# Performance work log

Measured on AMD Instinct MI355X. Metric: run time of the kernel, lower is better.

The kernel has to match this reference:

```python
import jax, jax.numpy as jnp
import numpy as np

N = 500_000      # total points
B = 64           # graphs in batch
D_IN = 64        # input feature dim (conv.in_tensor_reps.dim)
D_HID = 128      # EdgeConv MLP hidden
D_OUT = 128      # EdgeConv MLP out


def setup_inputs() -> dict:
    key = jax.random.key(0)
    k = jax.random.split(key, 8)
    x = jax.random.normal(k[0], (N, D_IN), jnp.float32)
    pos = jax.random.normal(k[1], (N, 3), jnp.float32)
    batch = jnp.sort(jax.random.randint(k[2], (N,), 0, B, dtype=jnp.int32))
    lframes = jax.random.normal(k[3], (N, 3, 3), jnp.float32)
    fan1 = 2 * D_IN + 3
    W1 = jax.random.normal(k[4], (fan1, D_HID), jnp.float32) / np.sqrt(fan1)
    b1 = jnp.zeros((D_HID,), jnp.float32)
    W2 = jax.random.normal(k[5], (D_HID, D_OUT), jnp.float32) / np.sqrt(D_HID)
    b2 = jnp.zeros((D_OUT,), jnp.float32)
    return {"x": x, "pos": pos, "batch": batch, "lframes": lframes,
            "W1": W1, "b1": b1, "W2": W2, "b2": b2}


def reference(x, pos, batch, lframes, W1, b1, W2, b2):
    n = pos.shape[0]
    # scatter-mean: center of mass per graph
    counts = jax.ops.segment_sum(jnp.ones((n,), pos.dtype), batch, num_segments=B)
    coms = jax.ops.segment_sum(pos, batch, num_segments=B) / jnp.maximum(counts, 1.0)[:, None]
    # distance of each point to its graph's COM
    dist = jnp.linalg.norm(pos - coms[batch], axis=-1)
    # scatter-min argmin per graph (first occurrence, like torch_scatter.scatter_min)
    min_d = jax.ops.segment_min(dist, batch, num_segments=B)
    node_ids = jnp.arange(n, dtype=jnp.int32)
    cand = jnp.where(dist <= min_d[batch], node_ids, n)
    idx = jnp.minimum(jax.ops.segment_min(cand, batch, num_segments=B), n - 1)  # [B]
    # gathers for the destination (center) nodes
    x_dst = x[idx]          # [B, D_IN]
    pos_dst = pos[idx]      # [B, 3]
    lframes_dst = lframes[idx]  # [B, 3, 3]
    # EdgeConv over edge_index = [arange(N) -> batch]:
    # message_e = MLP([x_dst_i, x_src_j - x_dst_i, pos_j - pos_i]), max-aggregated per graph
    xd = x_dst[batch]                      # [N, D_IN]
    feat = jnp.concatenate([xd, x - xd, pos - pos_dst[batch]], axis=-1)  # [N, 2*D_IN+3]
    h = jax.nn.relu(feat @ W1 + b1)        # [N, D_HID]
    msg = h @ W2 + b2                      # [N, D_OUT]
    out = jax.ops.segment_max(msg, batch, num_segments=B)  # [B, D_OUT]
    return out, pos_dst, batch[idx], lframes_dst
```

## Files before the change

### kernel.cpp

```cpp
#include <hip/hip_runtime.h>
#include <hip/hip_bf16.h>

#define NPTS 500000
#define NGR  64
#define TR   256
#define NT2  ((NPTS + TR - 1) / TR)
#define GRID2 256

typedef __bf16 bf16x8 __attribute__((ext_vector_type(8)));
typedef float f32x4 __attribute__((ext_vector_type(4)));
typedef unsigned int u32x4 __attribute__((ext_vector_type(4)));

#define OFF_DONE   4096
#define OFF_OUTACC 6144
#define OFF_CBIAS  38912
#define OFF_W1PT   71680
#define OFF_W1AT   73728
#define OFF_W2T    90112

__device__ __forceinline__ unsigned mapf(float f) {
    union { float f; unsigned u; } v; v.f = f;
    return ((int)v.u >= 0) ? (v.u | 0x80000000u) : ~v.u;
}

#define GLOAD_LDS16(g, l) __builtin_amdgcn_global_load_lds(                 \
    (__attribute__((address_space(1))) void*)(g),                           \
    (__attribute__((address_space(3))) void*)(l), 16, 0, 0)

__global__ __launch_bounds__(1024) void k_pre(
                      const float* __restrict__ pos,
                      const int* __restrict__ batch,
                      const float* __restrict__ x,
                      const float* __restrict__ W1,
                      const float* __restrict__ b1,
                      const float* __restrict__ W2,
                      const float* __restrict__ lfr,
                      unsigned short* __restrict__ W1aT,
                      unsigned short* __restrict__ W2T,
                      float* __restrict__ W1pT,
                      unsigned* __restrict__ outacc,
                      unsigned* __restrict__ done,
                      float* __restrict__ cbias,
                      float* __restrict__ outf) {
    __shared__ double sd[16][3];
    __shared__ unsigned long long sk[16];
    __shared__ double scom[3];
    __shared__ int sid;
    __shared__ float sposd[3];
    __shared__ float sp[4][128];
    __shared__ int sse[2];

    int g = blockIdx.x, t = threadIdx.x;
    int lane = t & 63, wv = t >> 6;

    {
        int i = g * 1024 + t;
        if (i == 0) *done = 0u;
        if (i < 8192) {
            outacc[i] = 0u;
            int n = i >> 6, k = i & 63;
            unsigned short v = (unsigned short)(__builtin_bit_cast(unsigned, (float)(__bf16)W1[(64 + k) * 128 + n]) >> 16);
            W1aT[i ^ ((n & 7) << 3)] = v;
        } else if (i < 8192 + 16384) {
            int j = i - 8192; int n = j >> 7, k = j & 127;
            unsigned short v = (unsigned short)(__builtin_bit_cast(unsigned, (float)(__bf16)W2[k * 128 + n]) >> 16);
            W2T[j ^ ((n & 7) << 3)] = v;
        } else if (i < 8192 + 16384 + 512) {
            int j = i - 24576; int n = j >> 2, q = j & 3;
            W1pT[j] = (q < 3) ? W1[(128 + q) * 128 + n] : 0.f;
        }
    }

    if (t < 2) {
        int target = g + t;
        int lo = 0, hi = NPTS;
        while (lo < hi) {
            int mid = (lo + hi) >> 1;
            if (batch[mid] < target) lo = mid + 1; else hi = mid;
        }
        sse[t] = lo;
    }
    __syncthreads();
    int s = sse[0], e = sse[1];

    double sx = 0.0, sy = 0.0, sz = 0.0;
    for (int i = s + t; i < e; i += 1024) {
        sx += (double)pos[i * 3 + 0];
        sy += (double)pos[i * 3 + 1];
        sz += (double)pos[i * 3 + 2];
    }
    #pragma unroll
    for (int m = 1; m < 64; m <<= 1) {
        sx += __shfl_xor(sx, m);
        sy += __shfl_xor(sy, m);
        sz += __shfl_xor(sz, m);
    }
    if (lane == 0) { sd[wv][0] = sx; sd[wv][1] = sy; sd[wv][2] = sz; }
    __syncthreads();
    if (t == 0) {
        double ax = 0.0, ay = 0.0, az = 0.0;
        for (int q = 0; q < 16; ++q) { ax += sd[q][0]; ay += sd[q][1]; az += sd[q][2]; }
        double cnt = (double)(e - s);
        double rc = 1.0 / (cnt > 1.0 ? cnt : 1.0);
        scom[0] = ax * rc; scom[1] = ay * rc; scom[2] = az * rc;
    }
    __syncthreads();
    double cx = scom[0], cy = scom[1], cz = scom[2];

    unsigned long long key = ~0ULL;
    for (int i = s + t; i < e; i += 1024) {
        double dx = (double)pos[i * 3 + 0] - cx;
        double dy = (double)pos[i * 3 + 1] - cy;
        double dz = (double)pos[i * 3 + 2] - cz;
        double d2 = __builtin_fma(dx, dx, __builtin_fma(dy, dy, dz * dz));
        unsigned long long b = __builtin_bit_cast(unsigned long long, d2);
        unsigned long long k2 = (b & ~0xFFFFFULL) | (unsigned long long)i;
        key = k2 < key ? k2 : key;
    }
    #pragma unroll
    for (int m = 1; m < 64; m <<= 1) {
        unsigned long long o = __shfl_xor(key, m);
        key = o < key ? o : key;
    }
    if (lane == 0) sk[wv] = key;
    __syncthreads();
    if (t == 0) {
        unsigned long long k = sk[0];
        for (int q = 1; q < 16; ++q) if (sk[q] < k) k = sk[q];
        int id = (int)(k & 0xFFFFFULL);
        if (id > NPTS - 1) id = NPTS - 1;
        sid = id;
    }
    __syncthreads();
    int id = sid;

    if (t < 3) {
        float p = pos[id * 3 + t];
        sposd[t] = p;
        outf[8192 + g * 3 + t] = p;
    }
    if (t == 4) outf[8192 + 192 + g] = (float)batch[id];
    if (t < 9) outf[8192 + 256 + g * 9 + t] = lfr[id * 9 + t];

    if (t < 512) {
        int c = t & 127, p = t >> 7;
        float part = 0.f;
        #pragma unroll
        for (int kq = 0; kq < 16; ++kq) {
            int k = p * 16 + kq;
            float xd = x[id * 64 + k];
            part += xd * (W1[k * 128 + c] - W1[(64 + k) * 128 + c]);
        }
        sp[p][c] = part;
    }
    __syncthreads();
    if (t < 128) {
        int c = t;
        float sv = b1[c] + sp[0][c] + sp[1][c] + sp[2][c] + sp[3][c];
        sv -= sposd[0] * W1[128 * 128 + c] + sposd[1] * W1[129 * 128 + c] + sposd[2] * W1[130 * 128 + c];
        cbias[g * 128 + c] = sv;
    }
}

__global__ __launch_bounds__(512, 2) void k_main(
    const float* __restrict__ x,
    const float* __restrict__ pos,
    const int* __restrict__ batch,
    const unsigned short* __restrict__ W1aT,
    const unsigned short* __restrict__ W2T,
    const float* __restrict__ W1pT,
    const float* __restrict__ cbias,
    unsigned* __restrict__ outacc,
    unsigned* __restrict__ done,
    const float* __restrict__ b2v,
    float* __restrict__ outf)
{
    __shared__ alignas(16) unsigned char smem[118784];
    __shared__ unsigned sflag;

    const int tid  = threadIdx.x;
    const int w    = tid >> 6;
    const int lane = tid & 63;
    const int quad = lane >> 4;
    const int mr   = lane & 15;

    #pragma unroll
    for (int i = 0; i < 2; ++i)
        GLOAD_LDS16((const char*)W1aT + (i * 512 + tid) * 16,
                    (char*)smem + (i * 512 + tid) * 16);
    #pragma unroll
    for (int i = 0; i < 4; ++i)
        GLOAD_LDS16((const char*)W2T + (i * 512 + tid) * 16,
                    (char*)smem + 16384 + (i * 512 + tid) * 16);

    bf16x8 bfrE[8];
    #pragma unroll
    for (int t8 = 0; t8 < 8; ++t8) {
        f32x4 wp = *(const f32x4*)(W1pT + (t8 * 16 + mr) * 4);
        bf16x8 e = (bf16x8){0, 0, 0, 0, 0, 0, 0, 0};
        if (quad == 0) { e[0] = (__bf16)wp[0]; e[1] = (__bf16)wp[1]; e[2] = (__bf16)wp[2]; }
        bfrE[t8] = e;
    }

    __syncthreads();

    const unsigned short* sW1 = (const unsigned short*)smem;
    const unsigned short* sW2 = (const unsigned short*)(smem + 16384);
    __bf16* hsb = (__bf16*)(smem + 49152) + w * 4352;
    const unsigned short* hss = (const unsigned short*)hsb;

    for (int t = blockIdx.x; t < NT2; t += GRID2) {
        const int row0 = t * TR + 32 * w;

        f32x4 av[2][4];
        #pragma unroll
        for (int u = 0; u < 2; ++u) {
            int gr2 = row0 + 16 * u + mr; if (gr2 > NPTS - 1) gr2 = NPTS - 1;
            const float* xp = x + (size_t)gr2 * 64 + quad * 8;
            av[u][0] = *(const f32x4*)(xp);
            av[u][1] = *(const f32x4*)(xp + 4);
            av[u][2] = *(const f32x4*)(xp + 32);
            av[u][3] = *(const f32x4*)(xp + 36);
        }

        int rowg[2][4]; bool rowv[2][4];
        #pragma unroll
        for (int u = 0; u < 2; ++u)
            #pragma unroll
            for (int r = 0; r < 4; ++r) {
                int gr = row0 + 16 * u + quad * 4 + r;
                rowv[u][r] = (gr < NPTS);
                rowg[u][r] = batch[gr < NPTS ? gr : NPTS - 1];
            }
        int gf = batch[row0 < NPTS ? row0 : NPTS - 1];
        int rl = row0 + 31; if (rl > NPTS - 1) rl = NPTS - 1;
        int gl = batch[rl];
        float cb0[8];
        #pragma unroll
        for (int t8 = 0; t8 < 8; ++t8) cb0[t8] = cbias[gf * 128 + t8 * 16 + mr];
        float pE[2][3];
        #pragma unroll
        for (int u = 0; u < 2; ++u) {
            int gp = row0 + 16 * u + mr; if (gp > NPTS - 1) gp = NPTS - 1;
            pE[u][0] = pos[gp * 3 + 0];
            pE[u][1] = pos[gp * 3 + 1];
            pE[u][2] = pos[gp * 3 + 2];
        }

        bf16x8 afr[2][2];
        #pragma unroll
        for (int u = 0; u < 2; ++u)
            #pragma unroll
            for (int h = 0; h < 2; ++h) {
                f32x4 va = av[u][2 * h], vb = av[u][2 * h + 1];
                bf16x8 a;
                a[0] = (__bf16)va[0]; a[1] = (__bf16)va[1]; a[2] = (__bf16)va[2]; a[3] = (__bf16)va[3];
                a[4] = (__bf16)vb[0]; a[5] = (__bf16)vb[1]; a[6] = (__bf16)vb[2]; a[7] = (__bf16)vb[3];
                afr[u][h] = a;
            }

        f32x4 acc[2][8];
        #pragma unroll
        for (int u = 0; u < 2; ++u)
            #pragma unroll
            for (int t8 = 0; t8 < 8; ++t8) acc[u][t8] = (f32x4){0.f, 0.f, 0.f, 0.f};
        #pragma unroll
        for (int t8 = 0; t8 < 8; ++t8) {
            int n = t8 * 16 + mr;
            int sw = (n & 7) << 3;
            bf16x8 bv0 = __builtin_bit_cast(bf16x8, *(const u32x4*)(sW1 + ((n * 64 + quad * 8) ^ sw)));
            bf16x8 bv1 = __builtin_bit_cast(bf16x8, *(const u32x4*)(sW1 + ((n * 64 + 32 + quad * 8) ^ sw)));
            #pragma unroll
            for (int u = 0; u < 2; ++u) {
                acc[u][t8] = __builtin_amdgcn_mfma_f32_16x16x32_bf16(afr[u][0], bv0, acc[u][t8], 0, 0, 0);
                acc[u][t8] = __builtin_amdgcn_mfma_f32_16x16x32_bf16(afr[u][1], bv1, acc[u][t8], 0, 0, 0);
            }
        }
        bf16x8 aE[2];
        #pragma unroll
        for (int u = 0; u < 2; ++u) {
            bf16x8 a = (bf16x8){0, 0, 0, 0, 0, 0, 0, 0};
            if (quad == 0) { a[0] = (__bf16)pE[u][0]; a[1] = (__bf16)pE[u][1]; a[2] = (__bf16)pE[u][2]; }
            aE[u] = a;
        }
        #pragma unroll
        for (int t8 = 0; t8 < 8; ++t8)
            #pragma unroll
            for (int u = 0; u < 2; ++u)
                acc[u][t8] = __builtin_amdgcn_mfma_f32_16x16x32_bf16(aE[u], bfrE[t8], acc[u][t8], 0, 0, 0);

        #pragma unroll
        for (int u = 0; u < 2; ++u)
            #pragma unroll
            for (int r = 0; r < 4; ++r) {
                int lrow = 16 * u + quad * 4 + r;
                int g = rowg[u][r];
                bool odd = (g != gf);
                #pragma unroll
                for (int t8 = 0; t8 < 8; ++t8) {
                    float cbv = cb0[t8];
                    if (odd) cbv = cbias[g * 128 + t8 * 16 + mr];
                    float v = fmaxf(acc[u][t8][r] + cbv, 0.f);
                    hsb[lrow * 136 + t8 * 16 + mr] = (__bf16)v;
                }
            }

        f32x4 acc2[2][8];
        #pragma unroll
        for (int u = 0; u < 2; ++u)
            #pragma unroll
            for (int t8 = 0; t8 < 8; ++t8) acc2[u][t8] = (f32x4){0.f, 0.f, 0.f, 0.f};
        #pragma unroll
        for (int kk = 0; kk < 4; ++kk) {
            bf16x8 a2[2];
            #pragma unroll
            for (int u = 0; u < 2; ++u)
                a2[u] = __builtin_bit_cast(bf16x8, *(const u32x4*)(hss + (16 * u + mr) * 136 + kk * 32 + quad * 8));
            #pragma unroll
            for (int t8 = 0; t8 < 8; ++t8) {
                int n = t8 * 16 + mr;
                bf16x8 bv = __builtin_bit_cast(bf16x8, *(const u32x4*)(sW2 + ((n * 128 + kk * 32 + quad * 8) ^ ((n & 7) << 3))));
                #pragma unroll
                for (int u = 0; u < 2; ++u)
                    acc2[u][t8] = __builtin_amdgcn_mfma_f32_16x16x32_bf16(a2[u], bv, acc2[u][t8], 0, 0, 0);
            }
        }

        for (int g = gf; g <= gl; ++g) {
            #pragma unroll
            for (int t8 = 0; t8 < 8; ++t8) {
                float m = -INFINITY;
                #pragma unroll
                for (int u = 0; u < 2; ++u)
                    #pragma unroll
                    for (int r = 0; r < 4; ++r)
                        if (rowv[u][r] && rowg[u][r] == g) m = fmaxf(m, acc2[u][t8][r]);
                m = fmaxf(m, __shfl_xor(m, 16));
                m = fmaxf(m, __shfl_xor(m, 32));
                unsigned mb = __builtin_bit_cast(unsigned, m);
                if (quad == 0 && mb != 0xFF800000u)
                    atomicMax(&outacc[g * 128 + t8 * 16 + mr], mapf(m));
            }
        }
    }

    __threadfence();
    __syncthreads();
    if (tid == 0) sflag = atomicAdd(done, 1u);
    __syncthreads();
    if (sflag == (unsigned)(gridDim.x - 1)) {
        for (int i = tid; i < 8192; i += 512) {
            unsigned key = atomicMax(&outacc[i], 0u);
            float v;
            if (key == 0u) {
                v = -300.f;
            } else {
                unsigned bits = (key & 0x80000000u) ? (key & 0x7FFFFFFFu) : ~key;
                union { unsigned u; float f; } c; c.u = bits; v = c.f;
            }
            outf[i] = v + b2v[i & 127];
        }
    }
}

extern "C" void kernel_launch(void* const* d_in, const int* in_sizes, int n_in,
                              void* d_out, int out_size, void* d_ws, size_t ws_size,
                              hipStream_t stream) {
    const float* x   = (const float*)d_in[0];
    const float* pos = (const float*)d_in[1];
    const int*   bat = (const int*)d_in[2];
    const float* lfr = (const float*)d_in[3];
    const float* W1  = (const float*)d_in[4];
    const float* b1  = (const float*)d_in[5];
    const float* W2  = (const float*)d_in[6];
    const float* b2v = (const float*)d_in[7];
    float* outf = (float*)d_out;

    char* ws = (char*)d_ws;
    unsigned*       done   = (unsigned*)(ws + OFF_DONE);
    unsigned*       outacc = (unsigned*)(ws + OFF_OUTACC);
    float*          cbias  = (float*)(ws + OFF_CBIAS);
    float*          W1pT   = (float*)(ws + OFF_W1PT);
    unsigned short* W1aT   = (unsigned short*)(ws + OFF_W1AT);
    unsigned short* W2T    = (unsigned short*)(ws + OFF_W2T);

    k_pre<<<64, 1024, 0, stream>>>(pos, bat, x, W1, b1, W2, lfr,
                                   W1aT, W2T, W1pT, outacc, done, cbias, outf);
    k_main<<<GRID2, 512, 0, stream>>>(x, pos, bat, W1aT, W2T, W1pT, cbias,
                                      outacc, done, b2v, outf);
}
```

Measured before the change: 320.8 us.

## Shrink LDS per block, double grid, and move finalization to separate kernel

The per-wave hidden-activation staging buffer now holds 16 rows with an XOR swizzle instead of 32 padded rows. The second GEMM is processed one 16-row half at a time, cutting LDS from about 116 KB to 80 KB so more blocks can be resident, and the grid doubles to 512. The last-block atomic counter finalization is replaced by a small separate output kernel, which removes the fence and atomic but adds a launch. The W1/W2 LDS loads are merged into one loop over the contiguous workspace, which assumes W2T directly follows W1aT.

```diff
diff --git a/kernel.cpp b/kernel.cpp
--- a/kernel.cpp
+++ b/kernel.cpp
@@ -5,13 +5,12 @@
 #define NGR  64
 #define TR   256
 #define NT2  ((NPTS + TR - 1) / TR)
-#define GRID2 256
+#define GRID2 512
 
 typedef __bf16 bf16x8 __attribute__((ext_vector_type(8)));
 typedef float f32x4 __attribute__((ext_vector_type(4)));
 typedef unsigned int u32x4 __attribute__((ext_vector_type(4)));
 
-#define OFF_DONE   4096
 #define OFF_OUTACC 6144
 #define OFF_CBIAS  38912
 #define OFF_W1PT   71680
@@ -39,7 +38,6 @@
                       unsigned short* __restrict__ W2T,
                       float* __restrict__ W1pT,
                       unsigned* __restrict__ outacc,
-                      unsigned* __restrict__ done,
                       float* __restrict__ cbias,
                       float* __restrict__ outf) {
     __shared__ double sd[16][3];
@@ -55,7 +53,6 @@
 
     {
         int i = g * 1024 + t;
-        if (i == 0) *done = 0u;
         if (i < 8192) {
             outacc[i] = 0u;
             int n = i >> 6, k = i & 63;
@@ -170,13 +167,9 @@
     const unsigned short* __restrict__ W2T,
     const float* __restrict__ W1pT,
     const float* __restrict__ cbias,
-    unsigned* __restrict__ outacc,
-    unsigned* __restrict__ done,
-    const float* __restrict__ b2v,
-    float* __restrict__ outf)
+    unsigned* __restrict__ outacc)
 {
-    __shared__ alignas(16) unsigned char smem[118784];
-    __shared__ unsigned sflag;
+    __shared__ alignas(16) unsigned char smem[81920];
 
     const int tid  = threadIdx.x;
     const int w    = tid >> 6;
@@ -185,13 +178,9 @@
     const int mr   = lane & 15;
 
     #pragma unroll
-    for (int i = 0; i < 2; ++i)
+    for (int i = 0; i < 6; ++i)
         GLOAD_LDS16((const char*)W1aT + (i * 512 + tid) * 16,
                     (char*)smem + (i * 512 + tid) * 16);
-    #pragma unroll
-    for (int i = 0; i < 4; ++i)
-        GLOAD_LDS16((const char*)W2T + (i * 512 + tid) * 16,
-                    (char*)smem + 16384 + (i * 512 + tid) * 16);
 
     bf16x8 bfrE[8];
     #pragma unroll
@@ -206,7 +195,7 @@
 
     const unsigned short* sW1 = (const unsigned short*)smem;
     const unsigned short* sW2 = (const unsigned short*)(smem + 16384);
-    __bf16* hsb = (__bf16*)(smem + 49152) + w * 4352;
+    __bf16* hsb = (__bf16*)(smem + 49152) + w * 2048;
     const unsigned short* hss = (const unsigned short*)hsb;
 
     for (int t = blockIdx.x; t < NT2; t += GRID2) {
@@ -289,40 +278,39 @@
             for (int u = 0; u < 2; ++u)
                 acc[u][t8] = __builtin_amdgcn_mfma_f32_16x16x32_bf16(aE[u], bfrE[t8], acc[u][t8], 0, 0, 0);
 
+        f32x4 acc2[2][8];
         #pragma unroll
         for (int u = 0; u < 2; ++u)
             #pragma unroll
+            for (int t8 = 0; t8 < 8; ++t8) acc2[u][t8] = (f32x4){0.f, 0.f, 0.f, 0.f};
+        #pragma unroll
+        for (int u = 0; u < 2; ++u) {
+            #pragma unroll
             for (int r = 0; r < 4; ++r) {
-                int lrow = 16 * u + quad * 4 + r;
+                int lrow = quad * 4 + r;
                 int g = rowg[u][r];
                 bool odd = (g != gf);
+                int sw = (lrow & 7) << 3;
                 #pragma unroll
                 for (int t8 = 0; t8 < 8; ++t8) {
                     float cbv = cb0[t8];
                     if (odd) cbv = cbias[g * 128 + t8 * 16 + mr];
                     float v = fmaxf(acc[u][t8][r] + cbv, 0.f);
-                    hsb[lrow * 136 + t8 * 16 + mr] = (__bf16)v;
+                    hsb[lrow * 128 + ((t8 * 16 + mr) ^ sw)] = (__bf16)v;
                 }
             }
-
-        f32x4 acc2[2][8];
-        #pragma unroll
-        for (int u = 0; u < 2; ++u)
-            #pragma unroll
-            for (int t8 = 0; t8 < 8; ++t8) acc2[u][t8] = (f32x4){0.f, 0.f, 0.f, 0.f};
-        #pragma unroll
-        for (int kk = 0; kk < 4; ++kk) {
-            bf16x8 a2[2];
-            #pragma unroll
-            for (int u = 0; u < 2; ++u)
-                a2[u] = __builtin_bit_cast(bf16x8, *(const u32x4*)(hss + (16 * u + mr) * 136 + kk * 32 + quad * 8));
-            #pragma unroll
-            for (int t8 = 0; t8 < 8; ++t8) {
-                int n = t8 * 16 + mr;
-                bf16x8 bv = __builtin_bit_cast(bf16x8, *(const u32x4*)(sW2 + ((n * 128 + kk * 32 + quad * 8) ^ ((n & 7) << 3))));
+            int swr = (mr & 7) << 3;
+            #pragma unroll
+            for (int kk = 0; kk < 4; ++kk) {
+                bf16x8 a2 = __builtin_bit_cast(bf16x8,
+                    *(const u32x4*)(hss + mr * 128 + ((kk * 32 + quad * 8) ^ swr)));
                 #pragma unroll
-                for (int u = 0; u < 2; ++u)
-                    acc2[u][t8] = __builtin_amdgcn_mfma_f32_16x16x32_bf16(a2[u], bv, acc2[u][t8], 0, 0, 0);
+                for (int t8 = 0; t8 < 8; ++t8) {
+                    int n = t8 * 16 + mr;
+                    bf16x8 bv = __builtin_bit_cast(bf16x8,
+                        *(const u32x4*)(sW2 + ((n * 128 + kk * 32 + quad * 8) ^ ((n & 7) << 3))));
+                    acc2[u][t8] = __builtin_amdgcn_mfma_f32_16x16x32_bf16(a2, bv, acc2[u][t8], 0, 0, 0);
+                }
             }
         }
 
@@ -343,24 +331,21 @@
             }
         }
     }
-
-    __threadfence();
-    __syncthreads();
-    if (tid == 0) sflag = atomicAdd(done, 1u);
-    __syncthreads();
-    if (sflag == (unsigned)(gridDim.x - 1)) {
-        for (int i = tid; i < 8192; i += 512) {
-            unsigned key = atomicMax(&outacc[i], 0u);
-            float v;
-            if (key == 0u) {
-                v = -300.f;
-            } else {
-                unsigned bits = (key & 0x80000000u) ? (key & 0x7FFFFFFFu) : ~key;
-                union { unsigned u; float f; } c; c.u = bits; v = c.f;
-            }
-            outf[i] = v + b2v[i & 127];
-        }
-    }
+}
+
+__global__ void k_out(const unsigned* __restrict__ outacc,
+                      const float* __restrict__ b2v,
+                      float* __restrict__ outf) {
+    int i = blockIdx.x * 256 + threadIdx.x;
+    unsigned key = outacc[i];
+    float v;
+    if (key == 0u) {
+        v = -300.f;
+    } else {
+        unsigned bits = (key & 0x80000000u) ? (key & 0x7FFFFFFFu) : ~key;
+        union { unsigned u; float f; } c; c.u = bits; v = c.f;
+    }
+    outf[i] = v + b2v[i & 127];
 }
 
 extern "C" void kernel_launch(void* const* d_in, const int* in_sizes, int n_in,
@@ -377,7 +362,6 @@
     float* outf = (float*)d_out;
 
     char* ws = (char*)d_ws;
-    unsigned*       done   = (unsigned*)(ws + OFF_DONE);
     unsigned*       outacc = (unsigned*)(ws + OFF_OUTACC);
     float*          cbias  = (float*)(ws + OFF_CBIAS);
     float*          W1pT   = (float*)(ws + OFF_W1PT);
@@ -385,7 +369,7 @@
     unsigned short* W2T    = (unsigned short*)(ws + OFF_W2T);
 
     k_pre<<<64, 1024, 0, stream>>>(pos, bat, x, W1, b1, W2, lfr,
-                                   W1aT, W2T, W1pT, outacc, done, cbias, outf);
-    k_main<<<GRID2, 512, 0, stream>>>(x, pos, bat, W1aT, W2T, W1pT, cbias,
-                                      outacc, done, b2v, outf);
-}
+                                   W1aT, W2T, W1pT, outacc, cbias, outf);
+    k_main<<<GRID2, 512, 0, stream>>>(x, pos, bat, W1aT, W2T, W1pT, cbias, outacc);
+    k_out<<<32, 256, 0, stream>>>(outacc, b2v, outf);
+}
```

Result: slower. 477.1 us (+48.7%).
